# Optimization experiments

Measured on AMD Instinct MI355X. Metric: run time of the kernel, lower is better.

Reference implementation:

```python
import jax, jax.numpy as jnp
import numpy as np

B, T, C, H = 2, 2048, 1024, 16
D = C // H  # d_head = 64


def setup_inputs() -> dict:
    key = jax.random.key(0)
    k1, k2, k3 = jax.random.split(key, 3)
    x = jax.random.normal(k1, (B, T, C), dtype=jnp.float32)
    # torch Linear weights stored pre-transposed as [in, out] so we apply x @ W
    w_qkv = jax.random.normal(k2, (C, 3 * C), dtype=jnp.float32) * (C ** -0.5)
    w_out = jax.random.normal(k3, (C, C), dtype=jnp.float32) * (C ** -0.5)
    charge_w = jnp.array([0.0, 3.0, 6.0], dtype=jnp.float32)  # CHARGES init
    # causal mask, broadcast over batch and heads; mask==0 positions are blocked
    mask = jnp.tril(jnp.ones((1, 1, T, T), dtype=jnp.int32))
    return {"x": x, "mask": mask, "w_qkv": w_qkv, "w_out": w_out, "charge_w": charge_w}


def reference(x, mask, w_qkv, w_out, charge_w):
    B, T, C = x.shape
    H = 16
    D = C // H
    qkv = (x @ w_qkv).reshape(B, T, 3, H, D)
    q, k, v = qkv[:, :, 0], qkv[:, :, 1], qkv[:, :, 2]  # each [B,T,H,D]
    scale = D ** -0.5
    attn = jnp.einsum("bqhd,bkhd->bhqk", q, k) * scale  # [B,H,T,T]
    charge_bias = jnp.mod(jnp.sum(charge_w), 9.0) * 0.001  # scalar bias
    attn = attn + charge_bias
    attn = jnp.where(mask == 0, jnp.float32(-1e9), attn)
    attn = jax.nn.softmax(attn, axis=-1)  # dropout is identity in eval mode
    out = jnp.einsum("bhqk,bkhd->bqhd", attn, v).reshape(B, T, C)
    return out @ w_out
```

## Files before the change

kernel.cpp:

```cpp
#include <hip/hip_runtime.h>
#include <stdint.h>


typedef __attribute__((ext_vector_type(4))) float f32x4;
typedef __attribute__((ext_vector_type(16))) float f32x16;
typedef __attribute__((ext_vector_type(8))) __bf16 bf16x8;
typedef __attribute__((ext_vector_type(8))) unsigned short ushort8;
typedef __attribute__((ext_vector_type(4))) unsigned short ushort4v;
typedef __attribute__((ext_vector_type(4))) unsigned int uint4v;

#define DEV __device__ __forceinline__

DEV unsigned short f32_to_bf16(float f) {
    union { float f; unsigned int u; } cv; cv.f = f;
    unsigned int u = cv.u;
    return (unsigned short)((u + 0x7FFFu + ((u >> 16) & 1u)) >> 16);
}

DEV float bf16_to_f32(unsigned short u) {
    union { unsigned int i; float f; } cv; cv.i = ((unsigned int)u) << 16;
    return cv.f;
}

DEV bf16x8 load_bf16x8(const unsigned short* p) {
    ushort8 v = *(const ushort8*)p;
    return __builtin_bit_cast(bf16x8, v);
}

DEV unsigned cvt_pk_bf16(float lo, float hi) {
    unsigned r;
    asm("v_cvt_pk_bf16_f32 %0, %1, %2" : "=v"(r) : "v"(lo), "v"(hi));
    return r;
}

DEV void gload_lds16(const void* g, void* l) {
    __builtin_amdgcn_global_load_lds(
        (const __attribute__((address_space(1))) unsigned int*)g,
        (__attribute__((address_space(3))) unsigned int*)l, 16, 0, 0);
}

DEV f32x16 vzero16() {
    f32x16 v;
#pragma unroll
    for (int i = 0; i < 16; ++i) v[i] = 0.f;
    return v;
}

DEV float tmax32(const f32x16& a, const f32x16& b) {
    float m[16];
#pragma unroll
    for (int i = 0; i < 16; ++i) m[i] = fmaxf(a[i], b[i]);
#pragma unroll
    for (int st = 8; st > 0; st >>= 1)
#pragma unroll
        for (int i = 0; i < 8; ++i) if (i < st) m[i] = fmaxf(m[i], m[i + st]);
    return m[0];
}
DEV float tsum32(const f32x16& a, const f32x16& b) {
    float m[16];
#pragma unroll
    for (int i = 0; i < 16; ++i) m[i] = a[i] + b[i];
#pragma unroll
    for (int st = 8; st > 0; st >>= 1)
#pragma unroll
        for (int i = 0; i < 8; ++i) if (i < st) m[i] = m[i] + m[i + st];
    return m[0];
}

__device__ __constant__ unsigned char qtab[24] = {15,15,7,14,14,13,13,6,12,12,11,11,5,10,10,9,9,4,8,8,3,2,1,0};
__device__ __constant__ unsigned char ctab[24] = {0,1,255,0,1,0,1,255,0,1,0,1,255,0,1,0,1,255,0,1,255,255,255,255};

__global__ void cvt_kernel(const float* __restrict__ in, unsigned short* __restrict__ out, int n) {
    int i = (blockIdx.x * blockDim.x + threadIdx.x) * 8;
    if (i >= n) return;
    f32x4 a = *(const f32x4*)(in + i);
    f32x4 b = *(const f32x4*)(in + i + 4);
    ushort8 o;
    o[0] = f32_to_bf16(a[0]); o[1] = f32_to_bf16(a[1]);
    o[2] = f32_to_bf16(a[2]); o[3] = f32_to_bf16(a[3]);
    o[4] = f32_to_bf16(b[0]); o[5] = f32_to_bf16(b[1]);
    o[6] = f32_to_bf16(b[2]); o[7] = f32_to_bf16(b[3]);
    *(ushort8*)(out + i) = o;
}

__global__ __launch_bounds__(256) void tcvt_kernel(const float* __restrict__ in,
                                                   unsigned short* __restrict__ out,
                                                   int R, int Cn) {
    __shared__ float tl[32][33];
    const int tx = threadIdx.x & 31, ty = threadIdx.x >> 5;
    const int c0 = blockIdx.x * 32, r0 = blockIdx.y * 32;
#pragma unroll
    for (int rr = 0; rr < 4; ++rr) {
        int r = ty + rr * 8;
        tl[r][tx] = in[(size_t)(r0 + r) * Cn + c0 + tx];
    }
    __syncthreads();
#pragma unroll
    for (int rr = 0; rr < 4; ++rr) {
        int cc = ty + rr * 8;
        out[(size_t)(c0 + cc) * R + r0 + tx] = f32_to_bf16(tl[tx][cc]);
    }
}

template<bool OUT_BF16, bool SCALE_Q>
__global__ __launch_bounds__(256) void gemm_kernel(
    const unsigned short* __restrict__ A,
    const unsigned short* __restrict__ Bt,
    void* __restrict__ C, int K, int ldc)
{
    __shared__ __align__(16) unsigned short As[3][4096];
    __shared__ __align__(16) unsigned short Bs[3][4096];

    const int tid = threadIdx.x;
    const int lane = tid & 63;
    const int w = tid >> 6;
    const int wr = w >> 1, wc = w & 1;
    const int g = lane >> 4, ci = lane & 15;
    const int bx = blockIdx.x, by = blockIdx.y;
    const int soff = w * 1024 + lane * 16;
    const int srow = soff >> 6;
    const int scch = (soff >> 4) & 3;

#define GSTAGE(buf, k0_) do { \
    _Pragma("unroll") for (int i_ = 0; i_ < 2; ++i_) { \
        int row_ = srow + i_ * 64; \
        gload_lds16(A  + (size_t)(by * 128 + row_) * K + (k0_) + scch * 8, \
                    (char*)As[buf] + i_ * 4096 + w * 1024); \
        gload_lds16(Bt + (size_t)(bx * 128 + row_) * K + (k0_) + scch * 8, \
                    (char*)Bs[buf] + i_ * 4096 + w * 1024); } } while (0)

    f32x4 acc[4][4];
#pragma unroll
    for (int i = 0; i < 4; ++i)
#pragma unroll
        for (int j = 0; j < 4; ++j) acc[i][j] = f32x4{0.f, 0.f, 0.f, 0.f};

    const int nk = K >> 5;
    GSTAGE(0, 0);
    GSTAGE(1, 32);
    asm volatile("s_waitcnt vmcnt(4)" ::: "memory");
    __builtin_amdgcn_sched_barrier(0);
    __builtin_amdgcn_s_barrier();
    __builtin_amdgcn_sched_barrier(0);

    for (int kt = 0; kt < nk; ++kt) {
        const int cur = kt % 3;
        if (kt + 2 < nk) GSTAGE((kt + 2) % 3, (kt + 2) << 5);

        bf16x8 af[4], bfr[4];
#pragma unroll
        for (int mf = 0; mf < 4; ++mf) af[mf]  = load_bf16x8(&As[cur][(wr * 64 + mf * 16 + ci) * 32 + g * 8]);
#pragma unroll
        for (int nf = 0; nf < 4; ++nf) bfr[nf] = load_bf16x8(&Bs[cur][(wc * 64 + nf * 16 + ci) * 32 + g * 8]);
        __builtin_amdgcn_s_setprio(1);
#pragma unroll
        for (int mf = 0; mf < 4; ++mf)
#pragma unroll
            for (int nf = 0; nf < 4; ++nf)
                acc[mf][nf] = __builtin_amdgcn_mfma_f32_16x16x32_bf16(af[mf], bfr[nf], acc[mf][nf], 0, 0, 0);
        __builtin_amdgcn_s_setprio(0);

        if (kt + 2 < nk) asm volatile("s_waitcnt vmcnt(4) lgkmcnt(0)" ::: "memory");
        else             asm volatile("s_waitcnt vmcnt(0) lgkmcnt(0)" ::: "memory");
        __builtin_amdgcn_sched_barrier(0);
        __builtin_amdgcn_s_barrier();
        __builtin_amdgcn_sched_barrier(0);
    }
#undef GSTAGE

#pragma unroll
    for (int mf = 0; mf < 4; ++mf)
#pragma unroll
        for (int nf = 0; nf < 4; ++nf)
#pragma unroll
            for (int r = 0; r < 4; ++r) {
                int row = by * 128 + wr * 64 + mf * 16 + g * 4 + r;
                int col = bx * 128 + wc * 64 + nf * 16 + ci;
                float v = acc[mf][nf][r];
                if (SCALE_Q && col < 1024) v *= 0.1803368801f;
                if (OUT_BF16)
                    ((unsigned short*)C)[(size_t)row * ldc + col] = f32_to_bf16(v);
                else
                    ((float*)C)[(size_t)row * ldc + col] = v;
            }
}

__global__ __launch_bounds__(256) void attn5_kernel(const unsigned short* __restrict__ qkv,
                                                    unsigned short* __restrict__ attn,
                                                    unsigned short* __restrict__ Obuf,
                                                    float* __restrict__ mlbuf) {
    constexpr int T = 2048, HD3 = 3072, Cc = 1024;
    __shared__ __align__(16) unsigned short Ks[3][4096];
    __shared__ __align__(16) unsigned short Vt[2][4096];

    const int tid = threadIdx.x;
    const int lane = tid & 63;
    const int w = tid >> 6;
    const int l31 = lane & 31;
    const int hi = lane >> 5;

    const int bx = blockIdx.x;
    const int j = bx >> 5;
    const int bh = bx & 31;
    const int q = qtab[j];
    const int ct = ctab[j];
    const int h = bh & 15;
    const int b = bh >> 4;
    const int q0w = q * 128 + w * 32;
    const int qrow = q0w + l31;
    const size_t base = (size_t)b * T * HD3;

    const int nt_full = 2 * q + 2;
    const int ts = (ct == 1) ? (q + 1) : 0;
    const int te = (ct == 0) ? (q + 1) : nt_full;
    const int ntc = te - ts;

    bf16x8 qf[4];
#pragma unroll
    for (int t = 0; t < 4; ++t)
        qf[t] = load_bf16x8(qkv + base + (size_t)qrow * HD3 + h * 64 + t * 16 + hi * 8);

    f32x16 acc0 = vzero16(), acc1 = vzero16();
    float m = -3e38f, l = 0.f;

    ushort8 vA0, vA1, vB0, vB1;
#define LOADV(tile, r0, r1) do { int kv0_ = (tile) * 64; \
    int rr0_ = tid >> 3, cc0_ = tid & 7; \
    r0 = *(const ushort8*)(qkv + base + (size_t)(kv0_ + rr0_) * HD3 + 2 * Cc + h * 64 + cc0_ * 8); \
    int c1_ = 256 + tid; int rr1_ = c1_ >> 3, cc1_ = c1_ & 7; \
    r1 = *(const ushort8*)(qkv + base + (size_t)(kv0_ + rr1_) * HD3 + 2 * Cc + h * 64 + cc1_ * 8); } while (0)

#define DMAK(tile, kb) do { int kv0_ = (tile) * 64; \
    _Pragma("unroll") for (int i_ = 0; i_ < 2; ++i_) { \
        int off_ = i_ * 4096 + w * 1024 + lane * 16; \
        int row_ = off_ >> 7; \
        int csw_ = ((lane & 7) * 8) ^ ((row_ & 7) * 8); \
        gload_lds16(qkv + base + (size_t)(kv0_ + row_) * HD3 + Cc + h * 64 + csw_, \
                    (void*)(((char*)&Ks[kb][0]) + i_ * 4096 + w * 1024)); } } while (0)

#define WRITEV(vb, r0, r1) do { \
    _Pragma("unroll") for (int i_ = 0; i_ < 2; ++i_) { \
        int c_ = i_ * 256 + tid; int row_ = c_ >> 3, cc_ = c_ & 7; \
        ushort8 v_ = i_ ? r1 : r0; \
        _Pragma("unroll") for (int j_ = 0; j_ < 8; ++j_) { \
            int d_ = cc_ * 8 + j_; \
            int sw_ = ((d_ ^ (d_ >> 3)) & 7) * 8; \
            Vt[vb][d_ * 64 + (row_ ^ sw_)] = v_[j_]; } } } while (0)

    LOADV(ts, vA0, vA1);
    DMAK(ts, 0);
    asm volatile("s_waitcnt vmcnt(0)" ::: "memory");
    __builtin_amdgcn_sched_barrier(0);
    WRITEV(0, vA0, vA1);
    LOADV(ts + 1, vB0, vB1);
    DMAK(ts + 1, 1);
    asm volatile("s_waitcnt lgkmcnt(0)" ::: "memory");
    __builtin_amdgcn_sched_barrier(0);
    __builtin_amdgcn_s_barrier();
    __builtin_amdgcn_sched_barrier(0);

    for (int tt = 0; tt < ntc; ++tt) {
        const int t = ts + tt;
        const int kv0 = t * 64;
        const int kcur = tt % 3;
        const int vcur = tt & 1;
        const bool act = (kv0 <= q0w + 31);
        const bool pre2 = (tt + 2) < ntc;

        if (tt + 1 < ntc) {
            if (tt & 1) WRITEV(vcur ^ 1, vA0, vA1); else WRITEV(vcur ^ 1, vB0, vB1);
        }
        if (pre2) {
            if (tt & 1) LOADV(t + 2, vB0, vB1); else LOADV(t + 2, vA0, vA1);
            DMAK(t + 2, (tt + 2) % 3);
        }

        if (act) {
            f32x16 s0 = vzero16(), s1 = vzero16();
            bf16x8 pf[4];
            const bool st1_ok = (kv0 + 32 <= q0w + 31);
            __builtin_amdgcn_s_setprio(1);
#pragma unroll
            for (int tf = 0; tf < 4; ++tf) {
                int row = l31;
                int idx = kcur * 4096 + row * 64 + ((tf * 16 + hi * 8) ^ ((row & 7) * 8));
                s0 = __builtin_amdgcn_mfma_f32_32x32x16_bf16(load_bf16x8(&Ks[0][idx]), qf[tf], s0, 0, 0, 0);
            }
            if (st1_ok) {
#pragma unroll
                for (int tf = 0; tf < 4; ++tf) {
                    int row = 32 + l31;
                    int idx = kcur * 4096 + row * 64 + ((tf * 16 + hi * 8) ^ ((row & 7) * 8));
                    s1 = __builtin_amdgcn_mfma_f32_32x32x16_bf16(load_bf16x8(&Ks[0][idx]), qf[tf], s1, 0, 0, 0);
                }
            }
            __builtin_amdgcn_s_setprio(0);
            const bool needmask = (kv0 + 63 > q0w);
            if (needmask) {
#pragma unroll
                for (int G = 0; G < 4; ++G)
#pragma unroll
                    for (int rr = 0; rr < 4; ++rr) {
                        int kvb = kv0 + 8 * G + 4 * hi + rr;
                        s0[G * 4 + rr] = (kvb      <= qrow) ? s0[G * 4 + rr] : -3e38f;
                        s1[G * 4 + rr] = (kvb + 32 <= qrow) ? s1[G * 4 + rr] : -3e38f;
                    }
            }
            float pmax = tmax32(s0, s1);
            pmax = fmaxf(pmax, __shfl_xor(pmax, 32));
            if (!__all(pmax - m <= 11.5f)) {
                float mnew = fmaxf(m, pmax);
                float alpha = exp2f(m - mnew);
                m = mnew;
                l *= alpha;
#pragma unroll
                for (int i = 0; i < 16; ++i) { acc0[i] *= alpha; acc1[i] *= alpha; }
            }
#pragma unroll
            for (int i = 0; i < 16; ++i) {
                s0[i] = exp2f(s0[i] - m);
                s1[i] = exp2f(s1[i] - m);
            }

            unsigned pk0[4][2], pk1[4][2];
#pragma unroll
            for (int G = 0; G < 4; ++G) {
                pk0[G][0] = cvt_pk_bf16(s0[G * 4 + 0], s0[G * 4 + 1]);
                pk0[G][1] = cvt_pk_bf16(s0[G * 4 + 2], s0[G * 4 + 3]);
                pk1[G][0] = cvt_pk_bf16(s1[G * 4 + 0], s1[G * 4 + 1]);
                pk1[G][1] = cvt_pk_bf16(s1[G * 4 + 2], s1[G * 4 + 3]);
            }
#pragma unroll
            for (int tf = 0; tf < 4; ++tf) {
                const int kb = tf & 1;
                unsigned sA0, sA1, sB0, sB1;
                if (tf < 2) { sA0 = pk0[2 * kb][0]; sA1 = pk0[2 * kb][1]; sB0 = pk0[2 * kb + 1][0]; sB1 = pk0[2 * kb + 1][1]; }
                else        { sA0 = pk1[2 * kb][0]; sA1 = pk1[2 * kb][1]; sB0 = pk1[2 * kb + 1][0]; sB1 = pk1[2 * kb + 1][1]; }
                unsigned sd0 = hi ? sA0 : sB0, sd1 = hi ? sA1 : sB1;
                unsigned rc0 = (unsigned)__shfl_xor((int)sd0, 32);
                unsigned rc1 = (unsigned)__shfl_xor((int)sd1, 32);
                uint4v u;
                u[0] = hi ? rc0 : sA0;  u[1] = hi ? rc1 : sA1;
                u[2] = hi ? sB0 : rc0;  u[3] = hi ? sB1 : rc1;
                pf[tf] = __builtin_bit_cast(bf16x8, u);
            }

            __builtin_amdgcn_s_setprio(1);
#pragma unroll
            for (int tf = 0; tf < 4; ++tf) {
                {
                    int d = l31, sw = ((d ^ (d >> 3)) & 7) * 8;
                    bf16x8 vf = load_bf16x8(&Vt[vcur][d * 64 + ((tf * 16 + hi * 8) ^ sw)]);
                    acc0 = __builtin_amdgcn_mfma_f32_32x32x16_bf16(vf, pf[tf], acc0, 0, 0, 0);
                }
                {
                    int d = 32 + l31, sw = ((d ^ (d >> 3)) & 7) * 8;
                    bf16x8 vf = load_bf16x8(&Vt[vcur][d * 64 + ((tf * 16 + hi * 8) ^ sw)]);
                    acc1 = __builtin_amdgcn_mfma_f32_32x32x16_bf16(vf, pf[tf], acc1, 0, 0, 0);
                }
            }
            __builtin_amdgcn_s_setprio(0);

            float rsum = tsum32(s0, s1);
            l += rsum + __shfl_xor(rsum, 32);
        }

        if (pre2) asm volatile("s_waitcnt vmcnt(4) lgkmcnt(0)" ::: "memory");
        else      asm volatile("s_waitcnt vmcnt(0) lgkmcnt(0)" ::: "memory");
        __builtin_amdgcn_sched_barrier(0);
        __builtin_amdgcn_s_barrier();
        __builtin_amdgcn_sched_barrier(0);
    }

    if (ct == 255) {
        const float invl = 1.0f / l;
        const size_t ob = (size_t)b * T * Cc + (size_t)qrow * Cc + h * 64;
#pragma unroll
        for (int G = 0; G < 4; ++G) {
            ushort4v o0, o1;
#pragma unroll
            for (int rr = 0; rr < 4; ++rr) {
                o0[rr] = f32_to_bf16(acc0[G * 4 + rr] * invl);
                o1[rr] = f32_to_bf16(acc1[G * 4 + rr] * invl);
            }
            int d0 = 8 * G + 4 * hi;
            *(ushort4v*)(attn + ob + d0) = o0;
            *(ushort4v*)(attn + ob + 32 + d0) = o1;
        }
    } else {
        const int slot = bh * 16 + (q - 8) * 2 + ct;
        const int qlocal = w * 32 + l31;
        unsigned short* op = Obuf + (size_t)slot * 8192 + qlocal * 64;
#pragma unroll
        for (int G = 0; G < 4; ++G) {
            ushort4v o0, o1;
#pragma unroll
            for (int rr = 0; rr < 4; ++rr) {
                o0[rr] = f32_to_bf16(acc0[G * 4 + rr]);
                o1[rr] = f32_to_bf16(acc1[G * 4 + rr]);
            }
            int d0 = 8 * G + 4 * hi;
            *(ushort4v*)(op + d0) = o0;
            *(ushort4v*)(op + 32 + d0) = o1;
        }
        if (hi == 0) {
            mlbuf[slot * 256 + qlocal * 2]     = m;
            mlbuf[slot * 256 + qlocal * 2 + 1] = l;
        }
    }
#undef LOADV
#undef DMAK
#undef WRITEV
}

__global__ __launch_bounds__(256) void combine_kernel(const unsigned short* __restrict__ Obuf,
                                                      const float* __restrict__ mlbuf,
                                                      unsigned short* __restrict__ attn) {
    constexpr int T = 2048, Cc = 1024;
    const int ss = blockIdx.x;
    const int bh = ss >> 3, qq = 8 + (ss & 7);
    const int b = bh >> 4, h = bh & 15;
    const int slot0 = bh * 16 + (qq - 8) * 2;
    const int tid = threadIdx.x;
    const int qlocal = tid >> 1, dh = (tid & 1) * 32;

    const float* ml0 = mlbuf + (size_t)slot0 * 256 + qlocal * 2;
    const float* ml1 = ml0 + 256;
    float m0 = ml0[0], l0 = ml0[1], m1 = ml1[0], l1 = ml1[1];
    float M = fmaxf(m0, m1);
    float w0 = exp2f(m0 - M), w1 = exp2f(m1 - M);
    float inv = 1.f / (w0 * l0 + w1 * l1);

    const unsigned short* p0 = Obuf + (size_t)slot0 * 8192 + qlocal * 64 + dh;
    const unsigned short* p1 = p0 + 8192;
    unsigned short* po = attn + (size_t)b * T * Cc + (size_t)(qq * 128 + qlocal) * Cc + h * 64 + dh;
#pragma unroll
    for (int i = 0; i < 4; ++i) {
        ushort8 a = *(const ushort8*)(p0 + i * 8);
        ushort8 c = *(const ushort8*)(p1 + i * 8);
        ushort8 o;
#pragma unroll
        for (int k = 0; k < 8; ++k)
            o[k] = f32_to_bf16((w0 * bf16_to_f32(a[k]) + w1 * bf16_to_f32(c[k])) * inv);
        *(ushort8*)(po + i * 8) = o;
    }
}

extern "C" void kernel_launch(void* const* d_in, const int* in_sizes, int n_in,
                              void* d_out, int out_size, void* d_ws, size_t ws_size,
                              hipStream_t stream) {
    const float* x     = (const float*)d_in[0];
    const float* w_qkv = (const float*)d_in[2];
    const float* w_out = (const float*)d_in[3];
    float* out = (float*)d_out;

    unsigned short* xb     = (unsigned short*)d_ws;
    unsigned short* wqkvT  = xb + 4194304;
    unsigned short* woutT  = wqkvT + 3145728;
    unsigned short* qkv    = woutT + 1048576;
    unsigned short* attn   = qkv + 12582912;
    unsigned short* Obuf   = xb;
    float*          mlbuf  = (float*)wqkvT;

    cvt_kernel<<<2048, 256, 0, stream>>>(x, xb, 4194304);
    tcvt_kernel<<<dim3(96, 32), 256, 0, stream>>>(w_qkv, wqkvT, 1024, 3072);
    tcvt_kernel<<<dim3(32, 32), 256, 0, stream>>>(w_out, woutT, 1024, 1024);

    gemm_kernel<true, true><<<dim3(24, 32), 256, 0, stream>>>(xb, wqkvT, (void*)qkv, 1024, 3072);

    attn5_kernel<<<768, 256, 0, stream>>>(qkv, attn, Obuf, mlbuf);
    combine_kernel<<<256, 256, 0, stream>>>(Obuf, mlbuf, attn);

    gemm_kernel<false, false><<<dim3(8, 32), 256, 0, stream>>>(attn, woutT, (void*)out, 1024, 1024);
}
```

Measured before the change: 141.8 us.

## Rebalance causal attention split-KV into finer chunks with multi-way combine

Replaces the two-way split of long query tiles with a table-driven schedule. Query tiles 5 through 15 are cut into 2 to 4 KV chunks of roughly equal length, which raises the block count from 768 to 1088. This is meant to even out per-block work and shrink the tail of the causal attention kernel. The first chunk writes unnormalized output directly into attn, and a generalized combine kernel merges up to four partials using their m/l stats. The cost is more partial-result traffic, a larger combine step, and hand-built lookup tables that must stay consistent.

```diff
diff --git a/kernel.cpp b/kernel.cpp
--- a/kernel.cpp
+++ b/kernel.cpp
@@ -67,8 +67,14 @@
     return m[0];
 }
 
-__device__ __constant__ unsigned char qtab[24] = {15,15,7,14,14,13,13,6,12,12,11,11,5,10,10,9,9,4,8,8,3,2,1,0};
-__device__ __constant__ unsigned char ctab[24] = {0,1,255,0,1,0,1,255,0,1,0,1,255,0,1,0,1,255,0,1,255,255,255,255};
+__device__ __constant__ unsigned char qA[34]  = {4,9,9,13,14,14,14, 8,8,12,12,13,13, 3,7,7,10,11,11,11,12,15,15,15,15, 6,6,10,10, 2,5,5, 1, 0};
+__device__ __constant__ unsigned char tsA[34] = {0,0,10,0,0,10,20, 0,9,0,9,10,19, 0,0,8,0,0,8,16,18,0,8,16,24, 0,7,8,15, 0,0,6, 0, 0};
+__device__ __constant__ unsigned char teA[34] = {10,10,20,10,10,20,30, 9,18,9,18,19,28, 8,8,16,8,8,16,24,26,8,16,24,32, 7,14,15,22, 6,6,12, 4, 2};
+__device__ __constant__ unsigned char mlA[34] = {255,8,9,19,22,23,24, 6,7,16,17,20,21, 255,4,5,10,13,14,15,18,25,26,27,28, 2,3,11,12, 255,0,1, 255, 255};
+__device__ __constant__ unsigned char obA[34] = {255,255,4,255,255,13,14, 255,3,255,9,11,12, 255,255,2,255,255,7,8,10,255,15,16,17, 255,1,5,6, 255,255,0, 255,255};
+__device__ __constant__ unsigned char ncs[11]  = {2,2,2,2,2,3,3,3,3,3,4};
+__device__ __constant__ unsigned char mlbs[11] = {0,2,4,6,8,10,13,16,19,22,25};
+__device__ __constant__ unsigned char obbs[11] = {0,1,2,3,4,5,7,9,11,13,15};
 
 __global__ void cvt_kernel(const float* __restrict__ in, unsigned short* __restrict__ out, int n) {
     int i = (blockIdx.x * blockDim.x + threadIdx.x) * 8;
@@ -185,7 +191,7 @@
             }
 }
 
-__global__ __launch_bounds__(256) void attn5_kernel(const unsigned short* __restrict__ qkv,
+__global__ __launch_bounds__(256) void attn6_kernel(const unsigned short* __restrict__ qkv,
                                                     unsigned short* __restrict__ attn,
                                                     unsigned short* __restrict__ Obuf,
                                                     float* __restrict__ mlbuf) {
@@ -202,17 +208,13 @@
     const int bx = blockIdx.x;
     const int j = bx >> 5;
     const int bh = bx & 31;
-    const int q = qtab[j];
-    const int ct = ctab[j];
+    const int q = qA[j];
+    const int ts = tsA[j], te = teA[j];
     const int h = bh & 15;
     const int b = bh >> 4;
     const int q0w = q * 128 + w * 32;
     const int qrow = q0w + l31;
     const size_t base = (size_t)b * T * HD3;
-
-    const int nt_full = 2 * q + 2;
-    const int ts = (ct == 1) ? (q + 1) : 0;
-    const int te = (ct == 0) ? (q + 1) : nt_full;
     const int ntc = te - ts;
 
     bf16x8 qf[4];
@@ -372,7 +374,8 @@
         __builtin_amdgcn_sched_barrier(0);
     }
 
-    if (ct == 255) {
+    const int mlq = mlA[j], obq = obA[j];
+    if (mlq == 255) {
         const float invl = 1.0f / l;
         const size_t ob = (size_t)b * T * Cc + (size_t)qrow * Cc + h * 64;
 #pragma unroll
@@ -388,9 +391,10 @@
             *(ushort4v*)(attn + ob + 32 + d0) = o1;
         }
     } else {
-        const int slot = bh * 16 + (q - 8) * 2 + ct;
         const int qlocal = w * 32 + l31;
-        unsigned short* op = Obuf + (size_t)slot * 8192 + qlocal * 64;
+        unsigned short* op = (obq == 255)
+            ? (attn + (size_t)b * T * Cc + (size_t)qrow * Cc + h * 64)
+            : (Obuf + (size_t)(bh * 18 + obq) * 8192 + qlocal * 64);
 #pragma unroll
         for (int G = 0; G < 4; ++G) {
             ushort4v o0, o1;
@@ -404,8 +408,8 @@
             *(ushort4v*)(op + 32 + d0) = o1;
         }
         if (hi == 0) {
-            mlbuf[slot * 256 + qlocal * 2]     = m;
-            mlbuf[slot * 256 + qlocal * 2 + 1] = l;
+            float* mp = mlbuf + (size_t)(bh * 29 + mlq) * 256 + qlocal * 2;
+            mp[0] = m; mp[1] = l;
         }
     }
 #undef LOADV
@@ -413,35 +417,57 @@
 #undef WRITEV
 }
 
-__global__ __launch_bounds__(256) void combine_kernel(const unsigned short* __restrict__ Obuf,
-                                                      const float* __restrict__ mlbuf,
-                                                      unsigned short* __restrict__ attn) {
+__global__ __launch_bounds__(256) void combine2_kernel(const unsigned short* __restrict__ Obuf,
+                                                       const float* __restrict__ mlbuf,
+                                                       unsigned short* __restrict__ attn) {
     constexpr int T = 2048, Cc = 1024;
     const int ss = blockIdx.x;
-    const int bh = ss >> 3, qq = 8 + (ss & 7);
+    const int bh = ss / 11, s = ss - bh * 11;
+    const int q = 5 + s;
+    const int nc = ncs[s], mlb = mlbs[s], obb = obbs[s];
     const int b = bh >> 4, h = bh & 15;
-    const int slot0 = bh * 16 + (qq - 8) * 2;
     const int tid = threadIdx.x;
     const int qlocal = tid >> 1, dh = (tid & 1) * 32;
 
-    const float* ml0 = mlbuf + (size_t)slot0 * 256 + qlocal * 2;
-    const float* ml1 = ml0 + 256;
-    float m0 = ml0[0], l0 = ml0[1], m1 = ml1[0], l1 = ml1[1];
-    float M = fmaxf(m0, m1);
-    float w0 = exp2f(m0 - M), w1 = exp2f(m1 - M);
-    float inv = 1.f / (w0 * l0 + w1 * l1);
-
-    const unsigned short* p0 = Obuf + (size_t)slot0 * 8192 + qlocal * 64 + dh;
-    const unsigned short* p1 = p0 + 8192;
-    unsigned short* po = attn + (size_t)b * T * Cc + (size_t)(qq * 128 + qlocal) * Cc + h * 64 + dh;
+    float mv[4], lv[4];
+#pragma unroll
+    for (int c = 0; c < 4; ++c) {
+        mv[c] = -3e38f; lv[c] = 0.f;
+        if (c < nc) {
+            const float* mp = mlbuf + (size_t)(bh * 29 + mlb + c) * 256 + qlocal * 2;
+            mv[c] = mp[0]; lv[c] = mp[1];
+        }
+    }
+    float M = fmaxf(fmaxf(mv[0], mv[1]), fmaxf(mv[2], mv[3]));
+    float fc[4];
+    float denom = 0.f;
+#pragma unroll
+    for (int c = 0; c < 4; ++c) {
+        fc[c] = (c < nc) ? exp2f(mv[c] - M) : 0.f;
+        denom += fc[c] * lv[c];
+    }
+    const float inv = 1.f / denom;
+#pragma unroll
+    for (int c = 0; c < 4; ++c) fc[c] *= inv;
+
+    unsigned short* po = attn + (size_t)b * T * Cc + (size_t)(q * 128 + qlocal) * Cc + h * 64 + dh;
 #pragma unroll
     for (int i = 0; i < 4; ++i) {
-        ushort8 a = *(const ushort8*)(p0 + i * 8);
-        ushort8 c = *(const ushort8*)(p1 + i * 8);
+        float acc[8] = {0.f, 0.f, 0.f, 0.f, 0.f, 0.f, 0.f, 0.f};
+#pragma unroll
+        for (int c = 0; c < 4; ++c) {
+            if (c < nc) {
+                const unsigned short* pc = (c == 0)
+                    ? po
+                    : (Obuf + (size_t)(bh * 18 + obb + c - 1) * 8192 + qlocal * 64 + dh);
+                ushort8 a = *(const ushort8*)(pc + i * 8);
+#pragma unroll
+                for (int k = 0; k < 8; ++k) acc[k] += fc[c] * bf16_to_f32(a[k]);
+            }
+        }
         ushort8 o;
 #pragma unroll
-        for (int k = 0; k < 8; ++k)
-            o[k] = f32_to_bf16((w0 * bf16_to_f32(a[k]) + w1 * bf16_to_f32(c[k])) * inv);
+        for (int k = 0; k < 8; ++k) o[k] = f32_to_bf16(acc[k]);
         *(ushort8*)(po + i * 8) = o;
     }
 }
@@ -460,7 +486,7 @@
     unsigned short* qkv    = woutT + 1048576;
     unsigned short* attn   = qkv + 12582912;
     unsigned short* Obuf   = xb;
-    float*          mlbuf  = (float*)wqkvT;
+    float*          mlbuf  = (float*)(xb + 4718592);
 
     cvt_kernel<<<2048, 256, 0, stream>>>(x, xb, 4194304);
     tcvt_kernel<<<dim3(96, 32), 256, 0, stream>>>(w_qkv, wqkvT, 1024, 3072);
@@ -468,8 +494,8 @@
 
     gemm_kernel<true, true><<<dim3(24, 32), 256, 0, stream>>>(xb, wqkvT, (void*)qkv, 1024, 3072);
 
-    attn5_kernel<<<768, 256, 0, stream>>>(qkv, attn, Obuf, mlbuf);
-    combine_kernel<<<256, 256, 0, stream>>>(Obuf, mlbuf, attn);
+    attn6_kernel<<<1088, 256, 0, stream>>>(qkv, attn, Obuf, mlbuf);
+    combine2_kernel<<<352, 256, 0, stream>>>(Obuf, mlbuf, attn);
 
     gemm_kernel<false, false><<<dim3(8, 32), 256, 0, stream>>>(attn, woutT, (void*)out, 1024, 1024);
 }
```

Measured after the change: 144.3 us. Within noise of the previous version (+1.8%).
